# Optimization experiments

Hardware: AMD Instinct MI355X
Metric: run time of the kernel (lower is better)

## Reference

```python
import jax, jax.numpy as jnp
import numpy as np

B, N, C, H = 2, 2048, 768, 12
HD = C // H
SCALE = HD ** -0.5


def setup_inputs() -> dict:
    key = jax.random.key(0)
    k1, k2, k3, k4 = jax.random.split(key, 4)
    return {
        "x": jax.random.normal(k1, (B, N, C), dtype=jnp.float32),
        "qkv_w": jax.random.normal(k2, (3 * C, C), dtype=jnp.float32) * (C ** -0.5),
        "proj_w": jax.random.normal(k3, (C, C), dtype=jnp.float32) * (C ** -0.5),
        "proj_b": jax.random.normal(k4, (C,), dtype=jnp.float32) * 0.01,
    }


def reference(x, qkv_w, proj_w, proj_b):
    b, n, c = x.shape
    # qkv: Linear(dim, 3*dim, bias=False) -> (B,N,3,H,HD) -> per-tensor (B,H,N,HD)
    qkv = (x @ qkv_w.T).reshape(b, n, 3, H, HD)
    q, k, v = jnp.moveaxis(qkv, 2, 0)          # each (B,N,H,HD)
    q = q.transpose(0, 2, 1, 3)                # (B,H,N,HD)
    k = k.transpose(0, 2, 1, 3)
    v = v.transpose(0, 2, 1, 3)
    attn_logits = jnp.einsum("bhqd,bhkd->bhqk", q, k) * SCALE  # (B,H,N,N)
    attn = jax.nn.softmax(attn_logits, axis=-1)
    score = jnp.mean(attn, axis=1)             # (B,N,N) mean over heads
    # dropout p=0.0 -> identity
    out = jnp.einsum("bhqk,bhkd->bhqd", attn, v)  # (B,H,N,HD)
    out = out.transpose(0, 2, 1, 3).reshape(b, n, c)
    out = out @ proj_w.T + proj_b
    return out, score
```

## Files before the change

### kernel.cpp

```cpp
#include <hip/hip_runtime.h>
#include <cstddef>

typedef __attribute__((ext_vector_type(8))) short bf16x8;
typedef __attribute__((ext_vector_type(4))) float f32x4;

constexpr int Bb = 2, Nn = 2048, Cc = 768, Hh = 12, HDd = 64;
constexpr float QSCALE = 0.125f * 1.44269504088896340736f;

__device__ inline short f2bf(float f) {
  unsigned u = __builtin_bit_cast(unsigned, f);
  u += 0x7fff + ((u >> 16) & 1);
  return (short)(u >> 16);
}
__device__ inline unsigned cvtpk(float a, float b) {
  unsigned r;
  asm("v_cvt_pk_bf16_f32 %0, %1, %2" : "=v"(r) : "v"(a), "v"(b));
  return r;
}
__device__ inline void gl_lds16(const void* g, void* l) {
  __builtin_amdgcn_global_load_lds(
      (const __attribute__((address_space(1))) unsigned*)g,
      (__attribute__((address_space(3))) unsigned*)l, 16, 0, 0);
}
__device__ inline bf16x8 lds8(const short* p) { return *(const bf16x8*)p; }
__device__ inline bf16x8 ld_frag(const short* base, int row, int ch) {
  return *(const bf16x8*)&base[row * 64 + (((ch ^ (row & 7)) << 3))];
}

__global__ __launch_bounds__(256) void cvt_kernel(const float* __restrict__ s,
                                                  short* __restrict__ d) {
  const int i = (blockIdx.x * 256 + threadIdx.x) * 4;
  const float4 v = *(const float4*)&s[i];
  short4 o;
  o.x = f2bf(v.x); o.y = f2bf(v.y); o.z = f2bf(v.z); o.w = f2bf(v.w);
  *(short4*)&d[i] = o;
}

__global__ __launch_bounds__(256) void qkv_mfma(
    const short* __restrict__ A, const short* __restrict__ W,
    short* __restrict__ Qg, short* __restrict__ Kg, short* __restrict__ Vtg) {
  __shared__ short As[128 * 64];
  __shared__ short Bs[128 * 64];
  const int t = threadIdx.x, l = t & 63, w = t >> 6;
  const int lr = l & 15, lh = l >> 4;
  const int m0 = blockIdx.x * 128, r0 = blockIdx.y * 128;
  const int wr = w >> 1, wc = w & 1;
  f32x4 acc[4][4];
#pragma unroll
  for (int i = 0; i < 4; ++i)
#pragma unroll
    for (int j = 0; j < 4; ++j) acc[i][j] = (f32x4){0.f, 0.f, 0.f, 0.f};

  for (int k0 = 0; k0 < Cc; k0 += 64) {
    __syncthreads();
#pragma unroll
    for (int u = 0; u < 4; ++u) {
      const int du = (w * 4 + u) * 64 + l;
      const int row = du >> 3, ch = du & 7, sch = ch ^ (row & 7);
      gl_lds16(A + (size_t)(m0 + row) * Cc + k0 + sch * 8,
               &As[(w * 4 + u) * 512]);
      gl_lds16(W + (size_t)(r0 + row) * Cc + k0 + sch * 8,
               &Bs[(w * 4 + u) * 512]);
    }
    __syncthreads();
#pragma unroll
    for (int kp = 0; kp < 2; ++kp) {
      bf16x8 af[4], bfv[4];
#pragma unroll
      for (int i = 0; i < 4; ++i)
        af[i] = ld_frag(As, wr * 64 + i * 16 + lr, kp * 4 + lh);
#pragma unroll
      for (int j = 0; j < 4; ++j)
        bfv[j] = ld_frag(Bs, wc * 64 + j * 16 + lr, kp * 4 + lh);
#pragma unroll
      for (int i = 0; i < 4; ++i)
#pragma unroll
        for (int j = 0; j < 4; ++j)
          acc[i][j] = __builtin_amdgcn_mfma_f32_16x16x32_bf16(
              af[i], bfv[j], acc[i][j], 0, 0, 0);
    }
  }
  const int which = r0 / Cc;
  const int rbase = r0 % Cc;
  const int bq = m0 >> 11;
  const int nb = (m0 & 2047) + wr * 64;
  if (which == 2) {
#pragma unroll
    for (int j = 0; j < 4; ++j) {
      const int rr = rbase + wc * 64 + j * 16 + lr;
      const int head = rr >> 6, dd = rr & 63;
      short* vp = &Vtg[(((size_t)bq * Hh + head) * HDd + dd) * Nn];
#pragma unroll
      for (int i = 0; i < 4; ++i) {
        short4 o;
        o.x = f2bf(acc[i][j][0]); o.y = f2bf(acc[i][j][1]);
        o.z = f2bf(acc[i][j][2]); o.w = f2bf(acc[i][j][3]);
        *(short4*)&vp[nb + i * 16 + lh * 4] = o;
      }
    }
  } else {
    const float scl = (which == 0) ? QSCALE : 1.0f;
    short* __restrict__ dst = (which == 0) ? Qg : Kg;
#pragma unroll
    for (int j = 0; j < 4; ++j) {
      const int rr = rbase + wc * 64 + j * 16 + lr;
      const int head = rr >> 6, dd = rr & 63;
      short* dp = &dst[((size_t)bq * Hh + head) * Nn * HDd + dd];
#pragma unroll
      for (int i = 0; i < 4; ++i)
#pragma unroll
        for (int r = 0; r < 4; ++r)
          dp[(size_t)(nb + i * 16 + lh * 4 + r) * HDd] =
              f2bf(acc[i][j][r] * scl);
    }
  }
}

__global__ __launch_bounds__(256, 3) void attn_pass1(
    const short* __restrict__ Qg, const short* __restrict__ Kg,
    const short* __restrict__ Vtg, float* __restrict__ Linv,
    short* __restrict__ OHb) {
  __shared__ short SM[2 * 8192 + 4 * 1024];
  __shared__ float LinvS[64];
  const int t = threadIdx.x, l = t & 63, w = t >> 6;
  const int lr = l & 15, lh = l >> 4;
  const int bid0 = blockIdx.x;
  const int bid = (bid0 & 7) * 96 + (bid0 >> 3);
  const int q0 = (bid & 31) * 64;
  const int head = (bid >> 5) % Hh;
  const int b = bid / (32 * Hh);
  const size_t base = (size_t)b * Hh + head;
  const short* Qh = Qg + base * Nn * HDd;
  const short* Kh = Kg + base * Nn * HDd;
  const short* Vh = Vtg + base * HDd * Nn;
  const int qw = q0 + w * 16;
  const int PB = 16384 + w * 1024;

  int fof[2][4], pof[2], wof[4];
#pragma unroll
  for (int kp = 0; kp < 2; ++kp) {
#pragma unroll
    for (int i = 0; i < 4; ++i)
      fof[kp][i] = (i * 16 + lr) * 64 + (((kp * 4 + lh) ^ (lr & 7)) << 3);
    pof[kp] = lr * 64 + (((kp * 4 + lh) ^ (lr & 7)) << 3);
  }
#pragma unroll
  for (int i = 0; i < 4; ++i) {
    const int ch = 2 * i + (lh >> 1);
    wof[i] = lr * 64 + ((ch ^ (lr & 7)) << 3) + (lh & 1) * 4;
  }

  bf16x8 qf[2];
#pragma unroll
  for (int kp = 0; kp < 2; ++kp)
    qf[kp] = *(const bf16x8*)&Qh[(size_t)(qw + lr) * HDd + kp * 32 + lh * 8];

  f32x4 accO[4];
#pragma unroll
  for (int j = 0; j < 4; ++j) accO[j] = (f32x4){0.f, 0.f, 0.f, 0.f};
  float Lp = 0.f;

  auto stage = [&](const int buf, const int tile) {
    const short* Kt = Kh + (size_t)tile * (64 * HDd);
    const short* Vt = Vh + tile * 64;
#pragma unroll
    for (int u = 0; u < 2; ++u) {
      const int du = (w * 2 + u) * 64 + l;
      const int row = du >> 3, ch = du & 7, sch = ch ^ (row & 7);
      gl_lds16(Kt + row * 64 + sch * 8, &SM[buf * 8192 + (w * 2 + u) * 512]);
      gl_lds16(Vt + (size_t)row * Nn + sch * 8,
               &SM[buf * 8192 + 4096 + (w * 2 + u) * 512]);
    }
  };

  auto compute = [&](const int kb) {
    f32x4 sacc[4];
#pragma unroll
    for (int i = 0; i < 4; ++i) sacc[i] = (f32x4){0.f, 0.f, 0.f, 0.f};
    __builtin_amdgcn_s_setprio(1);
#pragma unroll
    for (int kp = 0; kp < 2; ++kp)
#pragma unroll
      for (int i = 0; i < 4; ++i)
        sacc[i] = __builtin_amdgcn_mfma_f32_16x16x32_bf16(
            lds8(&SM[kb + fof[kp][i]]), qf[kp], sacc[i], 0, 0, 0);
    __builtin_amdgcn_s_setprio(0);
#pragma unroll
    for (int i = 0; i < 4; ++i) {
      const float p0 = exp2f(sacc[i][0]), p1 = exp2f(sacc[i][1]);
      const float p2 = exp2f(sacc[i][2]), p3 = exp2f(sacc[i][3]);
      Lp += (p0 + p1) + (p2 + p3);
      uint2 pk;
      pk.x = cvtpk(p0, p1);
      pk.y = cvtpk(p2, p3);
      *(uint2*)&SM[PB + wof[i]] = pk;
    }
    __builtin_amdgcn_s_setprio(1);
#pragma unroll
    for (int kp = 0; kp < 2; ++kp) {
      const bf16x8 pa = lds8(&SM[PB + pof[kp]]);
#pragma unroll
      for (int j = 0; j < 4; ++j)
        accO[j] = __builtin_amdgcn_mfma_f32_16x16x32_bf16(
            pa, lds8(&SM[kb + 4096 + fof[kp][j]]), accO[j], 0, 0, 0);
    }
    __builtin_amdgcn_s_setprio(0);
  };

  stage(0, 0);
  __syncthreads();
#pragma unroll 1
  for (int it = 0; it < Nn / 64; it += 2) {
    stage(1, it + 1);
    compute(0);
    __syncthreads();
    if (it + 2 < Nn / 64) stage(0, it + 2);
    compute(8192);
    __syncthreads();
  }

  Lp += __shfl_xor(Lp, 16, 64);
  Lp += __shfl_xor(Lp, 32, 64);
  const float linv = 1.0f / Lp;
  if (lh == 0) {
    Linv[base * Nn + qw + lr] = linv;
    LinvS[w * 16 + lr] = linv;
  }
  __syncthreads();
#pragma unroll
  for (int j = 0; j < 4; ++j) {
#pragma unroll
    for (int r = 0; r < 4; ++r) {
      const int ql = lh * 4 + r;
      const float li = LinvS[w * 16 + ql];
      OHb[((size_t)b * Nn + qw + ql) * Cc + head * HDd + j * 16 + lr] =
          f2bf(accO[j][r] * li);
    }
  }
}

__global__ __launch_bounds__(256, 4) void score_mfma(
    const short* __restrict__ Qg, const short* __restrict__ Kg,
    const float* __restrict__ Linv, float* __restrict__ score) {
  __shared__ short SM[2 * 8192];
  const int t = threadIdx.x, l = t & 63, w = t >> 6;
  const int lr = l & 15, lh = l >> 4;
  const int kv0 = blockIdx.x * 64, q0 = blockIdx.y * 64, b = blockIdx.z;
  const int qw = q0 + w * 16;

  int fof[2][4];
#pragma unroll
  for (int kp = 0; kp < 2; ++kp)
#pragma unroll
    for (int i = 0; i < 4; ++i)
      fof[kp][i] = (i * 16 + lr) * 64 + (((kp * 4 + lh) ^ (lr & 7)) << 3);

  f32x4 sc[4];
#pragma unroll
  for (int i = 0; i < 4; ++i) sc[i] = (f32x4){0.f, 0.f, 0.f, 0.f};

  auto stage = [&](const int buf, const int h) {
    const short* Kt = Kg + (((size_t)b * Hh + h) * Nn + kv0) * HDd;
    const short* Qt = Qg + (((size_t)b * Hh + h) * Nn + q0) * HDd;
#pragma unroll
    for (int u = 0; u < 2; ++u) {
      const int du = (w * 2 + u) * 64 + l;
      const int row = du >> 3, ch = du & 7, sch = ch ^ (row & 7);
      gl_lds16(Kt + row * 64 + sch * 8, &SM[buf * 8192 + (w * 2 + u) * 512]);
      gl_lds16(Qt + row * 64 + sch * 8,
               &SM[buf * 8192 + 4096 + (w * 2 + u) * 512]);
    }
  };

  auto compute = [&](const int kb, const int h) {
    const float linv = Linv[((size_t)b * Hh + h) * Nn + qw + lr];
    const bf16x8 q0f = lds8(&SM[kb + 4096 + fof[0][w]]);
    const bf16x8 q1f = lds8(&SM[kb + 4096 + fof[1][w]]);
    f32x4 sacc[4];
#pragma unroll
    for (int i = 0; i < 4; ++i) sacc[i] = (f32x4){0.f, 0.f, 0.f, 0.f};
    __builtin_amdgcn_s_setprio(1);
#pragma unroll
    for (int i = 0; i < 4; ++i)
      sacc[i] = __builtin_amdgcn_mfma_f32_16x16x32_bf16(
          lds8(&SM[kb + fof[0][i]]), q0f, sacc[i], 0, 0, 0);
#pragma unroll
    for (int i = 0; i < 4; ++i)
      sacc[i] = __builtin_amdgcn_mfma_f32_16x16x32_bf16(
          lds8(&SM[kb + fof[1][i]]), q1f, sacc[i], 0, 0, 0);
    __builtin_amdgcn_s_setprio(0);
#pragma unroll
    for (int i = 0; i < 4; ++i)
#pragma unroll
      for (int r = 0; r < 4; ++r) sc[i][r] += exp2f(sacc[i][r]) * linv;
  };

  stage(0, 0);
  __syncthreads();
#pragma unroll 1
  for (int h = 0; h < Hh; h += 2) {
    stage(1, h + 1);
    compute(0, h);
    __syncthreads();
    if (h + 2 < Hh) stage(0, h + 2);
    compute(8192, h + 1);
    __syncthreads();
  }

  constexpr float invH = 1.0f / 12.0f;
#pragma unroll
  for (int i = 0; i < 4; ++i) {
    f32x4 o;
#pragma unroll
    for (int r = 0; r < 4; ++r) o[r] = sc[i][r] * invH;
    *(f32x4*)&score[((size_t)b * Nn + qw + lr) * Nn + kv0 + i * 16 + lh * 4] =
        o;
  }
}

__global__ __launch_bounds__(256) void proj_mfma(
    const short* __restrict__ A, const short* __restrict__ W,
    const float* __restrict__ bias, float* __restrict__ out) {
  __shared__ short As[128 * 64];
  __shared__ short Bs[128 * 64];
  const int t = threadIdx.x, l = t & 63, w = t >> 6;
  const int lr = l & 15, lh = l >> 4;
  const int m0 = blockIdx.x * 128, c0 = blockIdx.y * 128;
  const int wr = w >> 1, wc = w & 1;
  f32x4 acc[4][4];
#pragma unroll
  for (int i = 0; i < 4; ++i)
#pragma unroll
    for (int j = 0; j < 4; ++j) acc[i][j] = (f32x4){0.f, 0.f, 0.f, 0.f};

  for (int k0 = 0; k0 < Cc; k0 += 64) {
    __syncthreads();
#pragma unroll
    for (int u = 0; u < 4; ++u) {
      const int du = (w * 4 + u) * 64 + l;
      const int row = du >> 3, ch = du & 7, sch = ch ^ (row & 7);
      gl_lds16(A + (size_t)(m0 + row) * Cc + k0 + sch * 8,
               &As[(w * 4 + u) * 512]);
      gl_lds16(W + (size_t)(c0 + row) * Cc + k0 + sch * 8,
               &Bs[(w * 4 + u) * 512]);
    }
    __syncthreads();
#pragma unroll
    for (int kp = 0; kp < 2; ++kp) {
      bf16x8 af[4], bfv[4];
#pragma unroll
      for (int i = 0; i < 4; ++i)
        af[i] = ld_frag(As, wr * 64 + i * 16 + lr, kp * 4 + lh);
#pragma unroll
      for (int j = 0; j < 4; ++j)
        bfv[j] = ld_frag(Bs, wc * 64 + j * 16 + lr, kp * 4 + lh);
#pragma unroll
      for (int i = 0; i < 4; ++i)
#pragma unroll
        for (int j = 0; j < 4; ++j)
          acc[i][j] = __builtin_amdgcn_mfma_f32_16x16x32_bf16(
              af[i], bfv[j], acc[i][j], 0, 0, 0);
    }
  }
#pragma unroll
  for (int j = 0; j < 4; ++j) {
    const int c = c0 + wc * 64 + j * 16 + lr;
    const float bi = bias[c];
#pragma unroll
    for (int i = 0; i < 4; ++i)
#pragma unroll
      for (int r = 0; r < 4; ++r) {
        const int m = m0 + wr * 64 + i * 16 + lh * 4 + r;
        out[(size_t)m * Cc + c] = acc[i][j][r] + bi;
      }
  }
}

extern "C" void kernel_launch(void* const* d_in, const int* in_sizes, int n_in,
                              void* d_out, int out_size, void* d_ws,
                              size_t ws_size, hipStream_t stream) {
  const float* x = (const float*)d_in[0];
  const float* qkv_w = (const float*)d_in[1];
  const float* proj_w = (const float*)d_in[2];
  const float* proj_b = (const float*)d_in[3];

  float* out = (float*)d_out;
  float* score = out + (size_t)Bb * Nn * Cc;

  const size_t nx = (size_t)Bb * Nn * Cc;
  const size_t nwq = (size_t)3 * Cc * Cc;
  const size_t npw = (size_t)Cc * Cc;
  short* xb = (short*)d_ws;
  short* wqb = xb + nx;
  short* pwb = wqb + nwq;
  short* Qb = pwb + npw;
  short* Kb = Qb + nx;
  short* Vtb = Kb + nx;
  short* OHb = Vtb + nx;
  float* Linv = (float*)(OHb + nx);

  cvt_kernel<<<dim3((int)(nx / 1024)), 256, 0, stream>>>(x, xb);
  cvt_kernel<<<dim3((int)(nwq / 1024)), 256, 0, stream>>>(qkv_w, wqb);
  cvt_kernel<<<dim3((int)(npw / 1024)), 256, 0, stream>>>(proj_w, pwb);
  qkv_mfma<<<dim3(32, 18), 256, 0, stream>>>(xb, wqb, Qb, Kb, Vtb);
  attn_pass1<<<dim3(Bb * Hh * 32), 256, 0, stream>>>(Qb, Kb, Vtb, Linv, OHb);
  score_mfma<<<dim3(32, 32, Bb), 256, 0, stream>>>(Qb, Kb, Linv, score);
  proj_mfma<<<dim3(32, 6), 256, 0, stream>>>(OHb, pwb, proj_b, out);
}
```

Baseline: 144.2 us.

## Give each wave two query tiles in attention and score kernels, and sum rows with MFMA

attn_pass1 now runs with 2 waves per block, each handling 32 query rows, so every K/V fragment read from LDS feeds two MFMAs. The softmax row sum moves from scalar adds plus cross-lane shuffles to an MFMA against a ones vector, which also drops the LDS round-trip for the inverse. score_mfma now covers 128 query rows per block, reads Q straight from global into registers with double buffering, stages only K in LDS, and remaps block ids with a swizzle. This cuts LDS traffic and repeated loads, but raises register pressure and gives fewer waves per block.

After: 196.0 us. 35.9% more time.

```diff
diff --git a/kernel.cpp b/kernel.cpp
--- a/kernel.cpp
+++ b/kernel.cpp
@@ -116,12 +116,11 @@
   }
 }
 
-__global__ __launch_bounds__(256, 3) void attn_pass1(
+__global__ __launch_bounds__(128, 2) void attn_pass1(
     const short* __restrict__ Qg, const short* __restrict__ Kg,
     const short* __restrict__ Vtg, float* __restrict__ Linv,
     short* __restrict__ OHb) {
-  __shared__ short SM[2 * 8192 + 4 * 1024];
-  __shared__ float LinvS[64];
+  __shared__ short SM[2 * 8192 + 2 * 2048];
   const int t = threadIdx.x, l = t & 63, w = t >> 6;
   const int lr = l & 15, lh = l >> 4;
   const int bid0 = blockIdx.x;
@@ -133,77 +132,103 @@
   const short* Qh = Qg + base * Nn * HDd;
   const short* Kh = Kg + base * Nn * HDd;
   const short* Vh = Vtg + base * HDd * Nn;
-  const int qw = q0 + w * 16;
-  const int PB = 16384 + w * 1024;
-
-  int fof[2][4], pof[2], wof[4];
-#pragma unroll
-  for (int kp = 0; kp < 2; ++kp) {
+  const int qw = q0 + w * 32;
+  const int PB = 16384 + w * 2048;
+
+  const bf16x8 onesf = {0x3F80, 0x3F80, 0x3F80, 0x3F80,
+                        0x3F80, 0x3F80, 0x3F80, 0x3F80};
+
+  int fof[2][4], pof[2][2], wof[2][4];
+#pragma unroll
+  for (int kp = 0; kp < 2; ++kp)
 #pragma unroll
     for (int i = 0; i < 4; ++i)
       fof[kp][i] = (i * 16 + lr) * 64 + (((kp * 4 + lh) ^ (lr & 7)) << 3);
-    pof[kp] = lr * 64 + (((kp * 4 + lh) ^ (lr & 7)) << 3);
-  }
-#pragma unroll
-  for (int i = 0; i < 4; ++i) {
-    const int ch = 2 * i + (lh >> 1);
-    wof[i] = lr * 64 + ((ch ^ (lr & 7)) << 3) + (lh & 1) * 4;
-  }
-
-  bf16x8 qf[2];
+#pragma unroll
+  for (int qi = 0; qi < 2; ++qi) {
+#pragma unroll
+    for (int kp = 0; kp < 2; ++kp)
+      pof[qi][kp] =
+          (qi * 16 + lr) * 64 + (((kp * 4 + lh) ^ (lr & 7)) << 3);
+#pragma unroll
+    for (int i = 0; i < 4; ++i) {
+      const int ch = 2 * i + (lh >> 1);
+      wof[qi][i] =
+          (qi * 16 + lr) * 64 + ((ch ^ (lr & 7)) << 3) + (lh & 1) * 4;
+    }
+  }
+
+  bf16x8 qf[2][2];
 #pragma unroll
   for (int kp = 0; kp < 2; ++kp)
-    qf[kp] = *(const bf16x8*)&Qh[(size_t)(qw + lr) * HDd + kp * 32 + lh * 8];
-
-  f32x4 accO[4];
-#pragma unroll
-  for (int j = 0; j < 4; ++j) accO[j] = (f32x4){0.f, 0.f, 0.f, 0.f};
-  float Lp = 0.f;
+#pragma unroll
+    for (int qi = 0; qi < 2; ++qi)
+      qf[kp][qi] = *(const bf16x8*)&Qh[(size_t)(qw + qi * 16 + lr) * HDd +
+                                       kp * 32 + lh * 8];
+
+  f32x4 accO[2][4], accL[2];
+#pragma unroll
+  for (int qi = 0; qi < 2; ++qi) {
+    accL[qi] = (f32x4){0.f, 0.f, 0.f, 0.f};
+#pragma unroll
+    for (int j = 0; j < 4; ++j) accO[qi][j] = (f32x4){0.f, 0.f, 0.f, 0.f};
+  }
 
   auto stage = [&](const int buf, const int tile) {
     const short* Kt = Kh + (size_t)tile * (64 * HDd);
     const short* Vt = Vh + tile * 64;
 #pragma unroll
-    for (int u = 0; u < 2; ++u) {
-      const int du = (w * 2 + u) * 64 + l;
+    for (int u = 0; u < 4; ++u) {
+      const int du = (u * 2 + w) * 64 + l;
       const int row = du >> 3, ch = du & 7, sch = ch ^ (row & 7);
-      gl_lds16(Kt + row * 64 + sch * 8, &SM[buf * 8192 + (w * 2 + u) * 512]);
+      gl_lds16(Kt + row * 64 + sch * 8, &SM[buf * 8192 + (u * 2 + w) * 512]);
       gl_lds16(Vt + (size_t)row * Nn + sch * 8,
-               &SM[buf * 8192 + 4096 + (w * 2 + u) * 512]);
+               &SM[buf * 8192 + 4096 + (u * 2 + w) * 512]);
     }
   };
 
   auto compute = [&](const int kb) {
-    f32x4 sacc[4];
-#pragma unroll
-    for (int i = 0; i < 4; ++i) sacc[i] = (f32x4){0.f, 0.f, 0.f, 0.f};
+    f32x4 sacc[4][2];
+#pragma unroll
+    for (int i = 0; i < 4; ++i)
+#pragma unroll
+      for (int qi = 0; qi < 2; ++qi) sacc[i][qi] = (f32x4){0.f, 0.f, 0.f, 0.f};
     __builtin_amdgcn_s_setprio(1);
 #pragma unroll
     for (int kp = 0; kp < 2; ++kp)
 #pragma unroll
-      for (int i = 0; i < 4; ++i)
-        sacc[i] = __builtin_amdgcn_mfma_f32_16x16x32_bf16(
-            lds8(&SM[kb + fof[kp][i]]), qf[kp], sacc[i], 0, 0, 0);
+      for (int i = 0; i < 4; ++i) {
+        const bf16x8 kf = lds8(&SM[kb + fof[kp][i]]);
+#pragma unroll
+        for (int qi = 0; qi < 2; ++qi)
+          sacc[i][qi] = __builtin_amdgcn_mfma_f32_16x16x32_bf16(
+              kf, qf[kp][qi], sacc[i][qi], 0, 0, 0);
+      }
     __builtin_amdgcn_s_setprio(0);
 #pragma unroll
-    for (int i = 0; i < 4; ++i) {
-      const float p0 = exp2f(sacc[i][0]), p1 = exp2f(sacc[i][1]);
-      const float p2 = exp2f(sacc[i][2]), p3 = exp2f(sacc[i][3]);
-      Lp += (p0 + p1) + (p2 + p3);
-      uint2 pk;
-      pk.x = cvtpk(p0, p1);
-      pk.y = cvtpk(p2, p3);
-      *(uint2*)&SM[PB + wof[i]] = pk;
-    }
+    for (int i = 0; i < 4; ++i)
+#pragma unroll
+      for (int qi = 0; qi < 2; ++qi) {
+        const float p0 = exp2f(sacc[i][qi][0]), p1 = exp2f(sacc[i][qi][1]);
+        const float p2 = exp2f(sacc[i][qi][2]), p3 = exp2f(sacc[i][qi][3]);
+        uint2 pk;
+        pk.x = cvtpk(p0, p1);
+        pk.y = cvtpk(p2, p3);
+        *(uint2*)&SM[PB + wof[qi][i]] = pk;
+      }
     __builtin_amdgcn_s_setprio(1);
 #pragma unroll
-    for (int kp = 0; kp < 2; ++kp) {
-      const bf16x8 pa = lds8(&SM[PB + pof[kp]]);
-#pragma unroll
-      for (int j = 0; j < 4; ++j)
-        accO[j] = __builtin_amdgcn_mfma_f32_16x16x32_bf16(
-            pa, lds8(&SM[kb + 4096 + fof[kp][j]]), accO[j], 0, 0, 0);
-    }
+    for (int kp = 0; kp < 2; ++kp)
+#pragma unroll
+      for (int qi = 0; qi < 2; ++qi) {
+        const bf16x8 pa = lds8(&SM[PB + pof[qi][kp]]);
+        accL[qi] = __builtin_amdgcn_mfma_f32_16x16x32_bf16(pa, onesf, accL[qi],
+                                                           0, 0, 0);
+#pragma unroll
+        for (int j = 0; j < 4; ++j)
+          accO[qi][j] = __builtin_amdgcn_mfma_f32_16x16x32_bf16(
+              pa, lds8(&SM[kb + 4096 + fof[kp][j]]), accO[qi][j], 0, 0, 0);
+      }
     __builtin_amdgcn_s_setprio(0);
   };
 
@@ -219,34 +244,34 @@
     __syncthreads();
   }
 
-  Lp += __shfl_xor(Lp, 16, 64);
-  Lp += __shfl_xor(Lp, 32, 64);
-  const float linv = 1.0f / Lp;
-  if (lh == 0) {
-    Linv[base * Nn + qw + lr] = linv;
-    LinvS[w * 16 + lr] = linv;
-  }
-  __syncthreads();
-#pragma unroll
-  for (int j = 0; j < 4; ++j) {
-#pragma unroll
-    for (int r = 0; r < 4; ++r) {
-      const int ql = lh * 4 + r;
-      const float li = LinvS[w * 16 + ql];
-      OHb[((size_t)b * Nn + qw + ql) * Cc + head * HDd + j * 16 + lr] =
-          f2bf(accO[j][r] * li);
-    }
+#pragma unroll
+  for (int qi = 0; qi < 2; ++qi) {
+    f32x4 linvq;
+#pragma unroll
+    for (int r = 0; r < 4; ++r) linvq[r] = 1.0f / accL[qi][r];
+    if (lr == 0)
+      *(f32x4*)&Linv[base * Nn + qw + qi * 16 + 4 * lh] = linvq;
+#pragma unroll
+    for (int j = 0; j < 4; ++j)
+#pragma unroll
+      for (int r = 0; r < 4; ++r)
+        OHb[((size_t)b * Nn + qw + qi * 16 + 4 * lh + r) * Cc + head * HDd +
+            j * 16 + lr] = f2bf(accO[qi][j][r] * linvq[r]);
   }
 }
 
 __global__ __launch_bounds__(256, 4) void score_mfma(
     const short* __restrict__ Qg, const short* __restrict__ Kg,
     const float* __restrict__ Linv, float* __restrict__ score) {
-  __shared__ short SM[2 * 8192];
+  __shared__ short SM[2 * 4096];
   const int t = threadIdx.x, l = t & 63, w = t >> 6;
   const int lr = l & 15, lh = l >> 4;
-  const int kv0 = blockIdx.x * 64, q0 = blockIdx.y * 64, b = blockIdx.z;
-  const int qw = q0 + w * 16;
+  const int raw = blockIdx.x;
+  const int nid = (raw & 7) * 128 + (raw >> 3);
+  const int kv0 = (nid & 31) * 64;
+  const int q0 = ((nid >> 5) & 15) * 128;
+  const int b = nid >> 9;
+  const int qw = q0 + w * 32;
 
   int fof[2][4];
 #pragma unroll
@@ -255,67 +280,94 @@
     for (int i = 0; i < 4; ++i)
       fof[kp][i] = (i * 16 + lr) * 64 + (((kp * 4 + lh) ^ (lr & 7)) << 3);
 
-  f32x4 sc[4];
-#pragma unroll
-  for (int i = 0; i < 4; ++i) sc[i] = (f32x4){0.f, 0.f, 0.f, 0.f};
+  f32x4 sc[4][2];
+#pragma unroll
+  for (int i = 0; i < 4; ++i)
+#pragma unroll
+    for (int qi = 0; qi < 2; ++qi) sc[i][qi] = (f32x4){0.f, 0.f, 0.f, 0.f};
 
   auto stage = [&](const int buf, const int h) {
     const short* Kt = Kg + (((size_t)b * Hh + h) * Nn + kv0) * HDd;
-    const short* Qt = Qg + (((size_t)b * Hh + h) * Nn + q0) * HDd;
 #pragma unroll
     for (int u = 0; u < 2; ++u) {
-      const int du = (w * 2 + u) * 64 + l;
+      const int du = (u * 4 + w) * 64 + l;
       const int row = du >> 3, ch = du & 7, sch = ch ^ (row & 7);
-      gl_lds16(Kt + row * 64 + sch * 8, &SM[buf * 8192 + (w * 2 + u) * 512]);
-      gl_lds16(Qt + row * 64 + sch * 8,
-               &SM[buf * 8192 + 4096 + (w * 2 + u) * 512]);
+      gl_lds16(Kt + row * 64 + sch * 8, &SM[buf * 4096 + (u * 4 + w) * 512]);
     }
   };
-
-  auto compute = [&](const int kb, const int h) {
-    const float linv = Linv[((size_t)b * Hh + h) * Nn + qw + lr];
-    const bf16x8 q0f = lds8(&SM[kb + 4096 + fof[0][w]]);
-    const bf16x8 q1f = lds8(&SM[kb + 4096 + fof[1][w]]);
-    f32x4 sacc[4];
-#pragma unroll
-    for (int i = 0; i < 4; ++i) sacc[i] = (f32x4){0.f, 0.f, 0.f, 0.f};
-    __builtin_amdgcn_s_setprio(1);
-#pragma unroll
-    for (int i = 0; i < 4; ++i)
-      sacc[i] = __builtin_amdgcn_mfma_f32_16x16x32_bf16(
-          lds8(&SM[kb + fof[0][i]]), q0f, sacc[i], 0, 0, 0);
-#pragma unroll
-    for (int i = 0; i < 4; ++i)
-      sacc[i] = __builtin_amdgcn_mfma_f32_16x16x32_bf16(
-          lds8(&SM[kb + fof[1][i]]), q1f, sacc[i], 0, 0, 0);
-    __builtin_amdgcn_s_setprio(0);
-#pragma unroll
-    for (int i = 0; i < 4; ++i)
-#pragma unroll
-      for (int r = 0; r < 4; ++r) sc[i][r] += exp2f(sacc[i][r]) * linv;
+  auto ldq = [&](bf16x8 qf[2][2], f32x4 lv[2], const int h) {
+    const size_t hb = (size_t)b * Hh + h;
+#pragma unroll
+    for (int kp = 0; kp < 2; ++kp)
+#pragma unroll
+      for (int qi = 0; qi < 2; ++qi)
+        qf[kp][qi] = *(const bf16x8*)&Qg[(hb * Nn + qw + qi * 16 + lr) * HDd +
+                                         kp * 32 + lh * 8];
+#pragma unroll
+    for (int qi = 0; qi < 2; ++qi)
+      lv[qi] = *(const f32x4*)&Linv[hb * Nn + qw + qi * 16 + 4 * lh];
   };
-
+  auto compute = [&](const int kb, const bf16x8 qf[2][2], const f32x4 lv[2]) {
+#pragma unroll
+    for (int ih = 0; ih < 4; ih += 2) {
+      f32x4 sacc[2][2];
+#pragma unroll
+      for (int ii = 0; ii < 2; ++ii)
+#pragma unroll
+        for (int qi = 0; qi < 2; ++qi)
+          sacc[ii][qi] = (f32x4){0.f, 0.f, 0.f, 0.f};
+      __builtin_amdgcn_s_setprio(1);
+#pragma unroll
+      for (int kp = 0; kp < 2; ++kp)
+#pragma unroll
+        for (int ii = 0; ii < 2; ++ii) {
+          const bf16x8 kf = lds8(&SM[kb + fof[kp][ih + ii]]);
+#pragma unroll
+          for (int qi = 0; qi < 2; ++qi)
+            sacc[ii][qi] = __builtin_amdgcn_mfma_f32_16x16x32_bf16(
+                kf, qf[kp][qi], sacc[ii][qi], 0, 0, 0);
+        }
+      __builtin_amdgcn_s_setprio(0);
+#pragma unroll
+      for (int ii = 0; ii < 2; ++ii)
+#pragma unroll
+        for (int qi = 0; qi < 2; ++qi)
+#pragma unroll
+          for (int r = 0; r < 4; ++r)
+            sc[ih + ii][qi][r] += exp2f(sacc[ii][qi][r]) * lv[qi][r];
+    }
+  };
+
+  bf16x8 qA[2][2], qB[2][2];
+  f32x4 lvA[2], lvB[2];
   stage(0, 0);
+  ldq(qA, lvA, 0);
   __syncthreads();
 #pragma unroll 1
   for (int h = 0; h < Hh; h += 2) {
     stage(1, h + 1);
-    compute(0, h);
-    __syncthreads();
-    if (h + 2 < Hh) stage(0, h + 2);
-    compute(8192, h + 1);
+    ldq(qB, lvB, h + 1);
+    compute(0, qA, lvA);
+    __syncthreads();
+    if (h + 2 < Hh) {
+      stage(0, h + 2);
+      ldq(qA, lvA, h + 2);
+    }
+    compute(4096, qB, lvB);
     __syncthreads();
   }
 
   constexpr float invH = 1.0f / 12.0f;
 #pragma unroll
-  for (int i = 0; i < 4; ++i) {
-    f32x4 o;
-#pragma unroll
-    for (int r = 0; r < 4; ++r) o[r] = sc[i][r] * invH;
-    *(f32x4*)&score[((size_t)b * Nn + qw + lr) * Nn + kv0 + i * 16 + lh * 4] =
-        o;
-  }
+  for (int i = 0; i < 4; ++i)
+#pragma unroll
+    for (int qi = 0; qi < 2; ++qi) {
+      f32x4 o;
+#pragma unroll
+      for (int r = 0; r < 4; ++r) o[r] = sc[i][qi][r] * invH;
+      *(f32x4*)&score[((size_t)b * Nn + qw + qi * 16 + lr) * Nn + kv0 +
+                      i * 16 + 4 * lh] = o;
+    }
 }
 
 __global__ __launch_bounds__(256) void proj_mfma(
@@ -403,7 +455,7 @@
   cvt_kernel<<<dim3((int)(nwq / 1024)), 256, 0, stream>>>(qkv_w, wqb);
   cvt_kernel<<<dim3((int)(npw / 1024)), 256, 0, stream>>>(proj_w, pwb);
   qkv_mfma<<<dim3(32, 18), 256, 0, stream>>>(xb, wqb, Qb, Kb, Vtb);
-  attn_pass1<<<dim3(Bb * Hh * 32), 256, 0, stream>>>(Qb, Kb, Vtb, Linv, OHb);
-  score_mfma<<<dim3(32, 32, Bb), 256, 0, stream>>>(Qb, Kb, Linv, score);
+  attn_pass1<<<dim3(Bb * Hh * 32), 128, 0, stream>>>(Qb, Kb, Vtb, Linv, OHb);
+  score_mfma<<<dim3(1024), 256, 0, stream>>>(Qb, Kb, Linv, score);
   proj_mfma<<<dim3(32, 6), 256, 0, stream>>>(OHb, pwb, proj_b, out);
 }
```

## Software-pipeline QK and PV across tiles, MFMA row sums, coalesce score stores

Applied to the files above, without the earlier changes.

The attention pass now splits K and V staging and runs the next tile's QK MFMAs alongside the current tile's exp and PV, so tensor-core work overlaps the exponent VALU work. Row sums come from an extra MFMA against a ones vector, which replaces the shuffle reduction and the LDS broadcast of the inverse. The score kernel reads Q fragments straight from global memory, pipelines QK across heads, remaps blocks per XCD for cache locality, and stages output through padded LDS so each row is written with coalesced stores. In exchange it uses more registers for the two in-flight score sets and adds an extra LDS pass and barrier at the end.

New measurement: 143.9 us. About the same (-0.2%).

```diff
diff --git a/kernel.cpp b/kernel.cpp
--- a/kernel.cpp
+++ b/kernel.cpp
@@ -120,12 +120,11 @@
     const short* __restrict__ Qg, const short* __restrict__ Kg,
     const short* __restrict__ Vtg, float* __restrict__ Linv,
     short* __restrict__ OHb) {
-  __shared__ short SM[2 * 8192 + 4 * 1024];
-  __shared__ float LinvS[64];
+  __shared__ short SM[4 * 4096 + 4 * 1024];
   const int t = threadIdx.x, l = t & 63, w = t >> 6;
   const int lr = l & 15, lh = l >> 4;
-  const int bid0 = blockIdx.x;
-  const int bid = (bid0 & 7) * 96 + (bid0 >> 3);
+  const int raw = blockIdx.x;
+  const int bid = (raw & 7) * 96 + (raw >> 3);
   const int q0 = (bid & 31) * 64;
   const int head = (bid >> 5) % Hh;
   const int b = bid / (32 * Hh);
@@ -136,7 +135,10 @@
   const int qw = q0 + w * 16;
   const int PB = 16384 + w * 1024;
 
-  int fof[2][4], pof[2], wof[4];
+  const bf16x8 onesf = {0x3F80, 0x3F80, 0x3F80, 0x3F80,
+                        0x3F80, 0x3F80, 0x3F80, 0x3F80};
+
+  int fof[2][4], wofi[4], pof[2];
 #pragma unroll
   for (int kp = 0; kp < 2; ++kp) {
 #pragma unroll
@@ -147,7 +149,7 @@
 #pragma unroll
   for (int i = 0; i < 4; ++i) {
     const int ch = 2 * i + (lh >> 1);
-    wof[i] = lr * 64 + ((ch ^ (lr & 7)) << 3) + (lh & 1) * 4;
+    wofi[i] = lr * 64 + ((ch ^ (lr & 7)) << 3) + (lh & 1) * 4;
   }
 
   bf16x8 qf[2];
@@ -155,97 +157,120 @@
   for (int kp = 0; kp < 2; ++kp)
     qf[kp] = *(const bf16x8*)&Qh[(size_t)(qw + lr) * HDd + kp * 32 + lh * 8];
 
-  f32x4 accO[4];
+  f32x4 accO[4], accL;
+  accL = (f32x4){0.f, 0.f, 0.f, 0.f};
 #pragma unroll
   for (int j = 0; j < 4; ++j) accO[j] = (f32x4){0.f, 0.f, 0.f, 0.f};
-  float Lp = 0.f;
-
-  auto stage = [&](const int buf, const int tile) {
+
+  auto stageK = [&](const int kb, const int tile) {
     const short* Kt = Kh + (size_t)tile * (64 * HDd);
+#pragma unroll
+    for (int u = 0; u < 2; ++u) {
+      const int cu = u * 4 + w;
+      const int du = cu * 64 + l;
+      const int row = du >> 3, ch = du & 7, sch = ch ^ (row & 7);
+      gl_lds16(Kt + row * 64 + sch * 8, &SM[kb + cu * 512]);
+    }
+  };
+  auto stageV = [&](const int vb, const int tile) {
     const short* Vt = Vh + tile * 64;
 #pragma unroll
     for (int u = 0; u < 2; ++u) {
-      const int du = (w * 2 + u) * 64 + l;
+      const int cu = u * 4 + w;
+      const int du = cu * 64 + l;
       const int row = du >> 3, ch = du & 7, sch = ch ^ (row & 7);
-      gl_lds16(Kt + row * 64 + sch * 8, &SM[buf * 8192 + (w * 2 + u) * 512]);
-      gl_lds16(Vt + (size_t)row * Nn + sch * 8,
-               &SM[buf * 8192 + 4096 + (w * 2 + u) * 512]);
-    }
-  };
-
-  auto compute = [&](const int kb) {
-    f32x4 sacc[4];
+      gl_lds16(Vt + (size_t)row * Nn + sch * 8, &SM[vb + cu * 512]);
+    }
+  };
+
+  auto qk = [&](const int kb, f32x4 (&sacc)[4]) {
 #pragma unroll
     for (int i = 0; i < 4; ++i) sacc[i] = (f32x4){0.f, 0.f, 0.f, 0.f};
-    __builtin_amdgcn_s_setprio(1);
 #pragma unroll
     for (int kp = 0; kp < 2; ++kp)
 #pragma unroll
       for (int i = 0; i < 4; ++i)
         sacc[i] = __builtin_amdgcn_mfma_f32_16x16x32_bf16(
             lds8(&SM[kb + fof[kp][i]]), qf[kp], sacc[i], 0, 0, 0);
-    __builtin_amdgcn_s_setprio(0);
+  };
+  auto expw = [&](const f32x4 (&sacc)[4]) {
 #pragma unroll
     for (int i = 0; i < 4; ++i) {
       const float p0 = exp2f(sacc[i][0]), p1 = exp2f(sacc[i][1]);
       const float p2 = exp2f(sacc[i][2]), p3 = exp2f(sacc[i][3]);
-      Lp += (p0 + p1) + (p2 + p3);
       uint2 pk;
       pk.x = cvtpk(p0, p1);
       pk.y = cvtpk(p2, p3);
-      *(uint2*)&SM[PB + wof[i]] = pk;
-    }
-    __builtin_amdgcn_s_setprio(1);
+      *(uint2*)&SM[PB + wofi[i]] = pk;
+    }
+  };
+  auto pv = [&](const int vb) {
 #pragma unroll
     for (int kp = 0; kp < 2; ++kp) {
       const bf16x8 pa = lds8(&SM[PB + pof[kp]]);
+      accL = __builtin_amdgcn_mfma_f32_16x16x32_bf16(pa, onesf, accL, 0, 0, 0);
 #pragma unroll
       for (int j = 0; j < 4; ++j)
         accO[j] = __builtin_amdgcn_mfma_f32_16x16x32_bf16(
-            pa, lds8(&SM[kb + 4096 + fof[kp][j]]), accO[j], 0, 0, 0);
-    }
-    __builtin_amdgcn_s_setprio(0);
-  };
-
-  stage(0, 0);
+            pa, lds8(&SM[vb + fof[kp][j]]), accO[j], 0, 0, 0);
+    }
+  };
+
+  f32x4 sA[4], sB[4];
+  stageK(0, 0);
+  __syncthreads();
+  stageK(4096, 1);
+  stageV(8192, 0);
+  qk(0, sA);
   __syncthreads();
 #pragma unroll 1
-  for (int it = 0; it < Nn / 64; it += 2) {
-    stage(1, it + 1);
-    compute(0);
-    __syncthreads();
-    if (it + 2 < Nn / 64) stage(0, it + 2);
-    compute(8192);
-    __syncthreads();
-  }
-
-  Lp += __shfl_xor(Lp, 16, 64);
-  Lp += __shfl_xor(Lp, 32, 64);
-  const float linv = 1.0f / Lp;
-  if (lh == 0) {
-    Linv[base * Nn + qw + lr] = linv;
-    LinvS[w * 16 + lr] = linv;
-  }
-  __syncthreads();
-#pragma unroll
-  for (int j = 0; j < 4; ++j) {
-#pragma unroll
-    for (int r = 0; r < 4; ++r) {
-      const int ql = lh * 4 + r;
-      const float li = LinvS[w * 16 + ql];
-      OHb[((size_t)b * Nn + qw + ql) * Cc + head * HDd + j * 16 + lr] =
-          f2bf(accO[j][r] * li);
-    }
-  }
+  for (int it = 1; it < 31; it += 2) {
+    stageK(0, it + 1);
+    stageV(12288, it);
+    qk(4096, sB);
+    expw(sA);
+    pv(8192);
+    __syncthreads();
+    stageK(4096, it + 2);
+    stageV(8192, it + 1);
+    qk(0, sA);
+    expw(sB);
+    pv(12288);
+    __syncthreads();
+  }
+  stageV(12288, 31);
+  qk(4096, sB);
+  expw(sA);
+  pv(8192);
+  __syncthreads();
+  expw(sB);
+  pv(12288);
+
+  f32x4 linvq;
+#pragma unroll
+  for (int r = 0; r < 4; ++r) linvq[r] = 1.0f / accL[r];
+  if (lr == 0) *(f32x4*)&Linv[base * Nn + qw + 4 * lh] = linvq;
+#pragma unroll
+  for (int j = 0; j < 4; ++j)
+#pragma unroll
+    for (int r = 0; r < 4; ++r)
+      OHb[((size_t)b * Nn + qw + 4 * lh + r) * Cc + head * HDd + j * 16 + lr] =
+          f2bf(accO[j][r] * linvq[r]);
 }
 
 __global__ __launch_bounds__(256, 4) void score_mfma(
     const short* __restrict__ Qg, const short* __restrict__ Kg,
     const float* __restrict__ Linv, float* __restrict__ score) {
-  __shared__ short SM[2 * 8192];
+  __shared__ __align__(16) char SMraw[64 * 68 * 4];
+  short* SK = (short*)SMraw;
+  float* SMf = (float*)SMraw;
   const int t = threadIdx.x, l = t & 63, w = t >> 6;
   const int lr = l & 15, lh = l >> 4;
-  const int kv0 = blockIdx.x * 64, q0 = blockIdx.y * 64, b = blockIdx.z;
+  const int raw = blockIdx.x;
+  const int xcd = raw & 7, idx = raw >> 3;
+  const int b = xcd >> 2;
+  const int q0 = ((xcd & 3) * 8 + (idx >> 5)) * 64;
+  const int kv0 = (idx & 31) * 64;
   const int qw = q0 + w * 16;
 
   int fof[2][4];
@@ -259,53 +284,72 @@
 #pragma unroll
   for (int i = 0; i < 4; ++i) sc[i] = (f32x4){0.f, 0.f, 0.f, 0.f};
 
-  auto stage = [&](const int buf, const int h) {
+  auto stage = [&](const int kb, const int h) {
     const short* Kt = Kg + (((size_t)b * Hh + h) * Nn + kv0) * HDd;
-    const short* Qt = Qg + (((size_t)b * Hh + h) * Nn + q0) * HDd;
 #pragma unroll
     for (int u = 0; u < 2; ++u) {
-      const int du = (w * 2 + u) * 64 + l;
+      const int cu = u * 4 + w;
+      const int du = cu * 64 + l;
       const int row = du >> 3, ch = du & 7, sch = ch ^ (row & 7);
-      gl_lds16(Kt + row * 64 + sch * 8, &SM[buf * 8192 + (w * 2 + u) * 512]);
-      gl_lds16(Qt + row * 64 + sch * 8,
-               &SM[buf * 8192 + 4096 + (w * 2 + u) * 512]);
-    }
-  };
-
-  auto compute = [&](const int kb, const int h) {
-    const float linv = Linv[((size_t)b * Hh + h) * Nn + qw + lr];
-    const bf16x8 q0f = lds8(&SM[kb + 4096 + fof[0][w]]);
-    const bf16x8 q1f = lds8(&SM[kb + 4096 + fof[1][w]]);
-    f32x4 sacc[4];
+      gl_lds16(Kt + row * 64 + sch * 8, &SK[kb + cu * 512]);
+    }
+  };
+  auto ldqQ = [&](const int h, bf16x8& a0, bf16x8& a1) {
+    const size_t hb = (size_t)b * Hh + h;
+    a0 = *(const bf16x8*)&Qg[(hb * Nn + qw + lr) * HDd + lh * 8];
+    a1 = *(const bf16x8*)&Qg[(hb * Nn + qw + lr) * HDd + 32 + lh * 8];
+  };
+  auto qk = [&](const int kb, const bf16x8 a0, const bf16x8 a1,
+                f32x4 (&sacc)[4]) {
 #pragma unroll
     for (int i = 0; i < 4; ++i) sacc[i] = (f32x4){0.f, 0.f, 0.f, 0.f};
-    __builtin_amdgcn_s_setprio(1);
 #pragma unroll
     for (int i = 0; i < 4; ++i)
       sacc[i] = __builtin_amdgcn_mfma_f32_16x16x32_bf16(
-          lds8(&SM[kb + fof[0][i]]), q0f, sacc[i], 0, 0, 0);
+          lds8(&SK[kb + fof[0][i]]), a0, sacc[i], 0, 0, 0);
 #pragma unroll
     for (int i = 0; i < 4; ++i)
       sacc[i] = __builtin_amdgcn_mfma_f32_16x16x32_bf16(
-          lds8(&SM[kb + fof[1][i]]), q1f, sacc[i], 0, 0, 0);
-    __builtin_amdgcn_s_setprio(0);
-#pragma unroll
-    for (int i = 0; i < 4; ++i)
-#pragma unroll
-      for (int r = 0; r < 4; ++r) sc[i][r] += exp2f(sacc[i][r]) * linv;
-  };
-
+          lds8(&SK[kb + fof[1][i]]), a1, sacc[i], 0, 0, 0);
+  };
+  auto expacc = [&](const f32x4 (&sacc)[4], const float lv) {
+#pragma unroll
+    for (int i = 0; i < 4; ++i)
+#pragma unroll
+      for (int r = 0; r < 4; ++r) sc[i][r] += exp2f(sacc[i][r]) * lv;
+  };
+
+  bf16x8 qA0, qA1, qB0, qB1;
+  float lvA, lvB;
+  f32x4 sA[4], sB[4];
   stage(0, 0);
+  ldqQ(0, qA0, qA1);
+  __syncthreads();
+  stage(4096, 1);
+  ldqQ(1, qB0, qB1);
+  lvA = Linv[((size_t)b * Hh + 0) * Nn + qw + lr];
+  qk(0, qA0, qA1, sA);
   __syncthreads();
 #pragma unroll 1
-  for (int h = 0; h < Hh; h += 2) {
-    stage(1, h + 1);
-    compute(0, h);
-    __syncthreads();
-    if (h + 2 < Hh) stage(0, h + 2);
-    compute(8192, h + 1);
-    __syncthreads();
-  }
+  for (int h = 1; h < 11; h += 2) {
+    stage(0, h + 1);
+    ldqQ(h + 1, qA0, qA1);
+    lvB = Linv[((size_t)b * Hh + h) * Nn + qw + lr];
+    qk(4096, qB0, qB1, sB);
+    expacc(sA, lvA);
+    __syncthreads();
+    stage(4096, h + 2);
+    ldqQ(h + 2, qB0, qB1);
+    lvA = Linv[((size_t)b * Hh + h + 1) * Nn + qw + lr];
+    qk(0, qA0, qA1, sA);
+    expacc(sB, lvB);
+    __syncthreads();
+  }
+  lvB = Linv[((size_t)b * Hh + 11) * Nn + qw + lr];
+  qk(4096, qB0, qB1, sB);
+  expacc(sA, lvA);
+  expacc(sB, lvB);
+  __syncthreads();
 
   constexpr float invH = 1.0f / 12.0f;
 #pragma unroll
@@ -313,8 +357,15 @@
     f32x4 o;
 #pragma unroll
     for (int r = 0; r < 4; ++r) o[r] = sc[i][r] * invH;
-    *(f32x4*)&score[((size_t)b * Nn + qw + lr) * Nn + kv0 + i * 16 + lh * 4] =
-        o;
+    *(f32x4*)&SMf[(w * 16 + lr) * 68 + i * 16 + 4 * lh] = o;
+  }
+  __syncthreads();
+#pragma unroll
+  for (int s = 0; s < 4; ++s) {
+    const int lin = t + s * 256;
+    const int row = lin >> 4, ch = lin & 15;
+    const f32x4 v = *(const f32x4*)&SMf[row * 68 + ch * 4];
+    *(f32x4*)&score[((size_t)b * Nn + q0 + row) * Nn + kv0 + ch * 4] = v;
   }
 }
 
@@ -403,7 +454,7 @@
   cvt_kernel<<<dim3((int)(nwq / 1024)), 256, 0, stream>>>(qkv_w, wqb);
   cvt_kernel<<<dim3((int)(npw / 1024)), 256, 0, stream>>>(proj_w, pwb);
   qkv_mfma<<<dim3(32, 18), 256, 0, stream>>>(xb, wqb, Qb, Kb, Vtb);
-  attn_pass1<<<dim3(Bb * Hh * 32), 256, 0, stream>>>(Qb, Kb, Vtb, Linv, OHb);
-  score_mfma<<<dim3(32, 32, Bb), 256, 0, stream>>>(Qb, Kb, Linv, score);
+  attn_pass1<<<dim3(768), 256, 0, stream>>>(Qb, Kb, Vtb, Linv, OHb);
+  score_mfma<<<dim3(2048), 256, 0, stream>>>(Qb, Kb, Linv, score);
   proj_mfma<<<dim3(32, 6), 256, 0, stream>>>(OHb, pwb, proj_b, out);
 }
```
